# Optimization experiments

Hardware: AMD Instinct MI355X
Metric: run time of the kernel (lower is better)

## Reference

```python
import jax, jax.numpy as jnp
import numpy as np

N, E = 50000, 800000
IN, HID, OUT, H = 128, 32, 32, 4
NEG_SLOPE = 0.2
EPS = 1e-5


def layernorm(x, g, b):
    mu = x.mean(-1, keepdims=True)
    var = ((x - mu) ** 2).mean(-1, keepdims=True)
    return (x - mu) * jax.lax.rsqrt(var + EPS) * g + b


def gat_conv(x, src, dst, W, a_s, a_d, bias, heads, ch, concat):
    n = x.shape[0]
    h = (x @ W).reshape(n, heads, ch)               # [N,H,C]
    alpha_s = (h * a_s).sum(-1)                     # [N,H]
    alpha_d = (h * a_d).sum(-1)                     # [N,H]
    e = jax.nn.leaky_relu(alpha_s[src] + alpha_d[dst], NEG_SLOPE)  # [E,H]
    m = jax.ops.segment_max(e, dst, num_segments=n)
    m = jnp.where(jnp.isfinite(m), m, 0.0)
    ex = jnp.exp(e - m[dst])
    denom = jax.ops.segment_sum(ex, dst, num_segments=n)
    alpha = ex / (denom[dst] + 1e-16)               # [E,H]
    msg = h[src] * alpha[:, :, None]                # [E,H,C]
    out = jax.ops.segment_sum(msg, dst, num_segments=n)  # [N,H,C]
    out = out.reshape(n, heads * ch) if concat else out.mean(axis=1)
    return out + bias


def setup_inputs() -> dict:
    key = jax.random.key(0)
    ks = jax.random.split(key, 24)
    HC = HID * H
    s = 0.05
    inp = {
        "x": jax.random.normal(ks[0], (N, IN), jnp.float32),
        "edge_index": jax.random.randint(ks[1], (2, E), 0, N),
        "W1": jax.random.normal(ks[2], (IN, HC), jnp.float32) * s,
        "as1": jax.random.normal(ks[3], (H, HID), jnp.float32) * s,
        "ad1": jax.random.normal(ks[4], (H, HID), jnp.float32) * s,
        "b1": jnp.zeros((HC,), jnp.float32),
        "g1": jnp.ones((HC,), jnp.float32),
        "be1": jnp.zeros((HC,), jnp.float32),
        "W2": jax.random.normal(ks[5], (HC, HC), jnp.float32) * s,
        "as2": jax.random.normal(ks[6], (H, HID), jnp.float32) * s,
        "ad2": jax.random.normal(ks[7], (H, HID), jnp.float32) * s,
        "b2": jnp.zeros((HC,), jnp.float32),
        "g2": jnp.ones((HC,), jnp.float32),
        "be2": jnp.zeros((HC,), jnp.float32),
        "W3": jax.random.normal(ks[8], (HC, OUT * H), jnp.float32) * s,
        "as3": jax.random.normal(ks[9], (H, OUT), jnp.float32) * s,
        "ad3": jax.random.normal(ks[10], (H, OUT), jnp.float32) * s,
        "b3": jnp.zeros((OUT,), jnp.float32),
        "Wsk": jax.random.normal(ks[11], (IN, HC), jnp.float32) * s,
        "bsk": jnp.zeros((HC,), jnp.float32),
    }
    return inp


def reference(x, edge_index, W1, as1, ad1, b1, g1, be1, W2, as2, ad2, b2, g2, be2, W3, as3, ad3, b3, Wsk, bsk):
    n = x.shape[0]
    loops = jnp.arange(n, dtype=edge_index.dtype)
    src = jnp.concatenate([edge_index[0], loops])
    dst = jnp.concatenate([edge_index[1], loops])
    h = gat_conv(x, src, dst, W1, as1, ad1, b1, H, HID, True)
    h = jax.nn.elu(h)
    h = layernorm(h, g1, be1)
    h = h + (x @ Wsk + bsk)  # residual (dropout is identity in eval)
    h = gat_conv(h, src, dst, W2, as2, ad2, b2, H, HID, True)
    h = jax.nn.elu(h)
    h = layernorm(h, g2, be2)
    h = gat_conv(h, src, dst, W3, as3, ad3, b3, H, OUT, False)
    return h
```

## Files before the change

### kernel.cpp

```cpp
#include <hip/hip_runtime.h>
#include <hip/hip_bf16.h>

typedef __attribute__((ext_vector_type(8))) short short8;
typedef __attribute__((ext_vector_type(4))) float f32x4;
using bf16 = __hip_bfloat16;

#define NEG_SLOPE 0.2f
#define LN_EPS 1e-5f

__device__ __forceinline__ unsigned short f2bfu(float v) {
    bf16 t = __float2bfloat16(v);
    unsigned short s;
    __builtin_memcpy(&s, &t, 2);
    return s;
}
__device__ __forceinline__ short f2bf(float v) {
    bf16 t = __float2bfloat16(v);
    short s;
    __builtin_memcpy(&s, &t, 2);
    return s;
}
__device__ __forceinline__ unsigned packbf(float a, float b) {
    return (unsigned)f2bfu(a) | ((unsigned)f2bfu(b) << 16);
}
__device__ __forceinline__ float bflo(unsigned u) { return __uint_as_float(u << 16); }
__device__ __forceinline__ float bfhi(unsigned u) { return __uint_as_float(u & 0xffff0000u); }
__device__ __forceinline__ float bf1(unsigned short u) { return __uint_as_float(((unsigned)u) << 16); }

__global__ void detect_k(const void* __restrict__ x, int* flag, int* bucketCnt) {
    int lane = threadIdx.x;
    for (int i = lane; i < 512; i += 64) bucketCnt[i] = 0;
    const unsigned short* u = (const unsigned short*)x;
    float m = 0.f;
    for (int i = lane; i < 8192; i += 64) {
        float v = fabsf(bf1(u[i]));
        if (!(v == v)) v = 1e30f;
        m = fmaxf(m, v);
    }
    for (int d = 1; d < 64; d <<= 1) m = fmaxf(m, __shfl_xor(m, d));
    if (lane == 0) flag[0] = (m > 1e4f) ? 1 : 0;
}

struct Ptr4 { const void* p[4]; };
struct Ptr14 { const void* p[14]; };
struct Ptr3 { const void* p[3]; };
struct Ptr6 { const void* p[6]; };
__global__ void stage_k(Ptr4 Ws, bf16* __restrict__ WT,
                        Ptr14 ptrs, bf16* __restrict__ sv,
                        Ptr3 Wv, Ptr6 av, bf16* __restrict__ vaT,
                        const int* __restrict__ flag) {
    int b = blockIdx.x;
    int f = flag[0];
    if (b < 256) {
        int gid = b * 256 + threadIdx.x;
        int m = gid >> 14;
        int idx = gid & 16383;
        int i = idx >> 7, j = idx & 127;
        const void* W = Ws.p[m];
        float v = f ? ((const float*)W)[idx]
                    : __bfloat162float(((const bf16*)W)[idx]);
        WT[m * 16384 + j * 128 + i] = __float2bfloat16(v);
    } else if (b == 256) {
        for (int k = threadIdx.x; k < 14 * 128; k += 256) {
            int t = k >> 7, i = k & 127;
            int n = (t == 12) ? 32 : 128;
            if (i < n) {
                const void* s = ptrs.p[t];
                float v = f ? ((const float*)s)[i]
                            : __bfloat162float(((const bf16*)s)[i]);
                sv[k] = __float2bfloat16(v);
            }
        }
    } else {
        int gid = (b - 257) * 256 + threadIdx.x;
        int l = gid >> 11;
        if (l >= 3) return;
        int c = (gid >> 7) & 15, k = gid & 127;
        float acc = 0.f;
        if (c < 8) {
            int hd = c & 3;
            const void* W = Wv.p[l];
            const void* a = av.p[l * 2 + (c >> 2)];
            for (int j = 0; j < 32; ++j) {
                float wv = f ? ((const float*)W)[k * 128 + hd * 32 + j]
                             : __bfloat162float(((const bf16*)W)[k * 128 + hd * 32 + j]);
                float avv = f ? ((const float*)a)[hd * 32 + j]
                              : __bfloat162float(((const bf16*)a)[hd * 32 + j]);
                acc += wv * avv;
            }
        }
        vaT[gid] = __float2bfloat16(acc);
    }
}

__global__ void bcount_k(const int* __restrict__ dst, int* bucketCnt, int E, int NB) {
    __shared__ int lc[512];
    int t = threadIdx.x;
    for (int i = t; i < NB; i += 256) lc[i] = 0;
    __syncthreads();
    int stride = gridDim.x * 256;
    for (int e = blockIdx.x * 256 + t; e < E; e += stride)
        atomicAdd(&lc[dst[e] >> 7], 1);
    __syncthreads();
    for (int i = t; i < NB; i += 256)
        if (lc[i]) atomicAdd(&bucketCnt[i], lc[i]);
}

__global__ void bscan_k(const int* __restrict__ bucketCnt, int* bucketOff,
                        int* bucketCur, int NB, int E) {
    int t = threadIdx.x;
    int v = (t < NB) ? bucketCnt[t] : 0;
    int incl = v;
    for (int d = 1; d < 64; d <<= 1) {
        int u = __shfl_up(incl, d);
        if ((t & 63) >= d) incl += u;
    }
    __shared__ int ws[8];
    if ((t & 63) == 63) ws[t >> 6] = incl;
    __syncthreads();
    int add = 0;
    for (int w = 0; w < (t >> 6); ++w) add += ws[w];
    int excl = incl - v + add;
    if (t < NB) { bucketOff[t] = excl; bucketCur[t] = excl; }
    if (t == 0) bucketOff[NB] = E;
}

#define SCAT_EPB 2048
__global__ __launch_bounds__(256) void bscatter_k(const int* __restrict__ src,
                                                  const int* __restrict__ dst,
                                                  int* bucketCur,
                                                  int* __restrict__ ebuf,
                                                  int E, int NB) {
    __shared__ int lcnt[512], lbase[512];
    int t = threadIdx.x;
    int e0 = blockIdx.x * SCAT_EPB;
    int cnt = E - e0;
    if (cnt > SCAT_EPB) cnt = SCAT_EPB;
    for (int i = t; i < NB; i += 256) lcnt[i] = 0;
    __syncthreads();
    for (int i = t; i < cnt; i += 256)
        atomicAdd(&lcnt[dst[e0 + i] >> 7], 1);
    __syncthreads();
    for (int i = t; i < NB; i += 256) {
        int c = lcnt[i];
        lbase[i] = c ? atomicAdd(&bucketCur[i], c) : 0;
        lcnt[i] = 0;
    }
    __syncthreads();
    for (int i = t; i < cnt; i += 256) {
        int d = dst[e0 + i];
        int b = d >> 7;
        int pos = lbase[b] + atomicAdd(&lcnt[b], 1);
        ebuf[pos] = ((d & 127) << 16) | src[e0 + i];
    }
}

__global__ __launch_bounds__(256) void build_k(const int* __restrict__ ebuf,
                                               const int* __restrict__ bucketOff,
                                               int* __restrict__ rowPtr,
                                               int* __restrict__ colSrc,
                                               int N, int E) {
    int b = blockIdx.x, t = threadIdx.x;
    int base = bucketOff[b];
    int cnt = bucketOff[b + 1] - base;
    __shared__ int nodeCnt[128], nodeCur[128], ws2[2];
    if (t < 128) nodeCnt[t] = 0;
    __syncthreads();
    for (int i = t; i < cnt; i += 256)
        atomicAdd(&nodeCnt[ebuf[base + i] >> 16], 1);
    __syncthreads();
    int v = 0, incl = 0;
    if (t < 128) {
        v = nodeCnt[t];
        incl = v;
        for (int d = 1; d < 64; d <<= 1) {
            int u = __shfl_up(incl, d);
            if ((t & 63) >= d) incl += u;
        }
        if ((t & 63) == 63) ws2[t >> 6] = incl;
    }
    __syncthreads();
    if (t < 128) {
        int excl = incl - v + ((t >= 64) ? ws2[0] : 0);
        int node = b * 128 + t;
        if (node < N) rowPtr[node] = base + excl;
        nodeCur[t] = excl;
    }
    if (b == 0 && t == 0) rowPtr[N] = E;
    __syncthreads();
    for (int i = t; i < cnt; i += 256) {
        int p = ebuf[base + i];
        int pos = base + atomicAdd(&nodeCur[p >> 16], 1);
        colSrc[pos] = (p & 0xffff) << 8;
    }
}

__global__ void hist_k(const int* __restrict__ dst, int* hist, int E) {
    int e = blockIdx.x * 256 + threadIdx.x;
    if (e < E) atomicAdd(&hist[dst[e]], 1);
}
__global__ void scanA_k(const int* __restrict__ hist, int* bsum, int N) {
    int i = blockIdx.x * 256 + threadIdx.x;
    int v = (i < N) ? hist[i] : 0;
    for (int d = 1; d < 64; d <<= 1) v += __shfl_xor(v, d);
    __shared__ int ws[4];
    if ((threadIdx.x & 63) == 0) ws[threadIdx.x >> 6] = v;
    __syncthreads();
    if (threadIdx.x == 0) bsum[blockIdx.x] = ws[0] + ws[1] + ws[2] + ws[3];
}
__global__ void scanB_k(const int* __restrict__ bsum, int* boff, int nb) {
    int t = threadIdx.x;
    int v = (t < nb) ? bsum[t] : 0;
    int incl = v;
    for (int d = 1; d < 64; d <<= 1) {
        int u = __shfl_up(incl, d);
        if ((t & 63) >= d) incl += u;
    }
    __shared__ int ws[4];
    if ((t & 63) == 63) ws[t >> 6] = incl;
    __syncthreads();
    int add = 0;
    for (int w = 0; w < (t >> 6); ++w) add += ws[w];
    if (t < nb) boff[t] = incl - v + add;
}
__global__ void scanC_k(const int* hist, const int* __restrict__ boff,
                        int* rowPtr, int* cursor, int N, int E) {
    int t = threadIdx.x;
    int i = blockIdx.x * 256 + t;
    int v = (i < N) ? hist[i] : 0;
    int incl = v;
    for (int d = 1; d < 64; d <<= 1) {
        int u = __shfl_up(incl, d);
        if ((t & 63) >= d) incl += u;
    }
    __shared__ int ws[4];
    if ((t & 63) == 63) ws[t >> 6] = incl;
    __syncthreads();
    int add = boff[blockIdx.x];
    for (int w = 0; w < (t >> 6); ++w) add += ws[w];
    int excl = incl - v + add;
    if (i < N) { rowPtr[i] = excl; cursor[i] = excl; }
    if (i == 0) rowPtr[N] = E;
}
__global__ void scatter_k(const int* __restrict__ src, const int* __restrict__ dst,
                          int* cursor, int* __restrict__ colSrc, int E) {
    int e = blockIdx.x * 256 + threadIdx.x;
    if (e >= E) return;
    int d = dst[e];
    int pos = atomicAdd(&cursor[d], 1);
    colSrc[pos] = src[e] << 8;
}

template <int DUAL>
__global__ __launch_bounds__(256) void gemm_k(const void* __restrict__ A,
                                              const bf16* __restrict__ WT,
                                              bf16* __restrict__ out0,
                                              bf16* __restrict__ out1,
                                              const bf16* __restrict__ bias1,
                                              const bf16* __restrict__ vaT,
                                              float* __restrict__ asN,
                                              float* __restrict__ adN,
                                              int N, const int* __restrict__ flag) {
    int wave = threadIdx.x >> 6, lane = threadIdx.x & 63;
    int lm = lane & 15, lk = lane >> 4;
    int rowBase = blockIdx.x * 32;
    const short* Ws = (const short*)WT;
    const short* Vs = (const short*)vaT;
    bool f32m = flag && flag[0];

    short8 bw0[2][4], bw1[DUAL ? 2 : 1][DUAL ? 4 : 1];
#pragma unroll
    for (int ct = 0; ct < 2; ++ct) {
        int c = (wave * 2 + ct) * 16 + lm;
#pragma unroll
        for (int kk = 0; kk < 4; ++kk)
            bw0[ct][kk] = *(const short8*)(Ws + (size_t)c * 128 + kk * 32 + lk * 8);
    }
    if (DUAL) {
#pragma unroll
        for (int ct = 0; ct < 2; ++ct) {
            int c = (wave * 2 + ct) * 16 + lm;
#pragma unroll
            for (int kk = 0; kk < 4; ++kk)
                bw1[ct][kk] = *(const short8*)(Ws + 16384 + (size_t)c * 128 + kk * 32 + lk * 8);
        }
    }
    short8 va8[4];
    if (wave == 0) {
#pragma unroll
        for (int kk = 0; kk < 4; ++kk)
            va8[kk] = *(const short8*)(Vs + (size_t)lm * 128 + kk * 32 + lk * 8);
    }

    short8 af[2][4];
#pragma unroll
    for (int rt = 0; rt < 2; ++rt) {
        int r = rowBase + rt * 16 + lm;
        if (r >= N) r = N - 1;
        if (f32m) {
#pragma unroll
            for (int kk = 0; kk < 4; ++kk) {
                const float* Af = (const float*)A + (size_t)r * 128 + kk * 32 + lk * 8;
                float4 q0 = *(const float4*)(Af);
                float4 q1 = *(const float4*)(Af + 4);
                short8 v;
                v[0] = f2bf(q0.x); v[1] = f2bf(q0.y); v[2] = f2bf(q0.z); v[3] = f2bf(q0.w);
                v[4] = f2bf(q1.x); v[5] = f2bf(q1.y); v[6] = f2bf(q1.z); v[7] = f2bf(q1.w);
                af[rt][kk] = v;
            }
        } else {
#pragma unroll
            for (int kk = 0; kk < 4; ++kk)
                af[rt][kk] = *(const short8*)((const short*)A + (size_t)r * 128 + kk * 32 + lk * 8);
        }
    }

    f32x4 acc0[2][2];
    f32x4 acc1[DUAL ? 2 : 1][DUAL ? 2 : 1];
#pragma unroll
    for (int ct = 0; ct < 2; ++ct)
#pragma unroll
        for (int rt = 0; rt < 2; ++rt) acc0[ct][rt] = (f32x4){0.f, 0.f, 0.f, 0.f};
    if (DUAL) {
#pragma unroll
        for (int ct = 0; ct < 2; ++ct)
#pragma unroll
            for (int rt = 0; rt < 2; ++rt) acc1[ct][rt] = (f32x4){0.f, 0.f, 0.f, 0.f};
    }

#pragma unroll
    for (int rt = 0; rt < 2; ++rt) {
#pragma unroll
        for (int kk = 0; kk < 4; ++kk) {
            acc0[0][rt] = __builtin_amdgcn_mfma_f32_16x16x32_bf16(af[rt][kk], bw0[0][kk], acc0[0][rt], 0, 0, 0);
            acc0[1][rt] = __builtin_amdgcn_mfma_f32_16x16x32_bf16(af[rt][kk], bw0[1][kk], acc0[1][rt], 0, 0, 0);
            if (DUAL) {
                acc1[0][rt] = __builtin_amdgcn_mfma_f32_16x16x32_bf16(af[rt][kk], bw1[0][kk], acc1[0][rt], 0, 0, 0);
                acc1[1][rt] = __builtin_amdgcn_mfma_f32_16x16x32_bf16(af[rt][kk], bw1[1][kk], acc1[1][rt], 0, 0, 0);
            }
        }
    }

#pragma unroll
    for (int ct = 0; ct < 2; ++ct) {
        int c = (wave * 2 + ct) * 16 + lm;
#pragma unroll
        for (int rt = 0; rt < 2; ++rt) {
#pragma unroll
            for (int i = 0; i < 4; ++i) {
                int r = rowBase + rt * 16 + lk * 4 + i;
                if (r < N) out0[(size_t)r * 128 + c] = __float2bfloat16(acc0[ct][rt][i]);
            }
        }
    }
    if (DUAL) {
#pragma unroll
        for (int ct = 0; ct < 2; ++ct) {
            int c = (wave * 2 + ct) * 16 + lm;
            float bv = __bfloat162float(bias1[c]);
#pragma unroll
            for (int rt = 0; rt < 2; ++rt) {
#pragma unroll
                for (int i = 0; i < 4; ++i) {
                    int r = rowBase + rt * 16 + lk * 4 + i;
                    if (r < N) out1[(size_t)r * 128 + c] = __float2bfloat16(acc1[ct][rt][i] + bv);
                }
            }
        }
    }

    if (wave == 0) {
        f32x4 accA[2];
#pragma unroll
        for (int rt = 0; rt < 2; ++rt) accA[rt] = (f32x4){0.f, 0.f, 0.f, 0.f};
#pragma unroll
        for (int rt = 0; rt < 2; ++rt)
#pragma unroll
            for (int kk = 0; kk < 4; ++kk)
                accA[rt] = __builtin_amdgcn_mfma_f32_16x16x32_bf16(af[rt][kk], va8[kk], accA[rt], 0, 0, 0);
        if (lm < 8) {
            float* dst = (lm < 4) ? asN : adN;
            int hh = lm & 3;
#pragma unroll
            for (int rt = 0; rt < 2; ++rt)
#pragma unroll
                for (int i = 0; i < 4; ++i) {
                    int r = rowBase + rt * 16 + lk * 4 + i;
                    if (r < N) dst[(size_t)r * 4 + hh] = accA[rt][i];
                }
        }
    }
}

template <int MODE>
__global__ __launch_bounds__(256) void agg_k(const bf16* __restrict__ h,
                                             const float* __restrict__ asN,
                                             const float* __restrict__ adN,
                                             const int* __restrict__ rowPtr,
                                             const int* __restrict__ colSrc,
                                             const bf16* __restrict__ bvec,
                                             const bf16* __restrict__ g,
                                             const bf16* __restrict__ be,
                                             void* outv, int N, int E,
                                             const int* __restrict__ flag) {
    int wv = threadIdx.x >> 6, lane = threadIdx.x & 63;
    int n = blockIdx.x * 4 + wv;
    if (n >= N) return;
    int grp = lane >> 4, t = lane & 15;
    int hd = t >> 2;
    const char* hbase = (const char*)h + t * 16;
    const char* abase = (const char*)asN + hd * 4;

    uint4 hself = *(const uint4*)(hbase + (size_t)n * 256);
    float adn = adN[(size_t)n * 4 + hd];
    float asn_self = asN[(size_t)n * 4 + hd];

    float a[8];
#pragma unroll
    for (int k = 0; k < 8; ++k) a[k] = 0.f;
    float den = 0.f;

    int st = rowPtr[n], en = rowPtr[n + 1];
    if ((unsigned)st > (unsigned)E) st = 0;
    if ((unsigned)en > (unsigned)E) en = st;
    if (en < st) en = st;

    int j = st + grp;
    int off = (j < en) ? colSrc[j] : 0;
    float av = *(const float*)(abase + (off >> 4));
    uint4 hq = *(const uint4*)(hbase + off);
    for (; j < en; j += 4) {
        int off2 = colSrc[j + 4];
        float av2 = *(const float*)(abase + (off2 >> 4));
        uint4 hq2 = *(const uint4*)(hbase + off2);
        float e = av + adn;
        float w = __expf(fmaxf(e, NEG_SLOPE * e));
        den += w;
        a[0] += w * bflo(hq.x); a[1] += w * bfhi(hq.x);
        a[2] += w * bflo(hq.y); a[3] += w * bfhi(hq.y);
        a[4] += w * bflo(hq.z); a[5] += w * bfhi(hq.z);
        a[6] += w * bflo(hq.w); a[7] += w * bfhi(hq.w);
        av = av2; hq = hq2;
    }

#pragma unroll
    for (int k = 0; k < 8; ++k) {
        a[k] += __shfl_xor(a[k], 16);
        a[k] += __shfl_xor(a[k], 32);
    }
    den += __shfl_xor(den, 16);
    den += __shfl_xor(den, 32);

    float es = asn_self + adn;
    float wsf = __expf(fmaxf(es, NEG_SLOPE * es));
    den += wsf;
    a[0] += wsf * bflo(hself.x); a[1] += wsf * bfhi(hself.x);
    a[2] += wsf * bflo(hself.y); a[3] += wsf * bfhi(hself.y);
    a[4] += wsf * bflo(hself.z); a[5] += wsf * bfhi(hself.z);
    a[6] += wsf * bflo(hself.w); a[7] += wsf * bfhi(hself.w);

    float inv = 1.f / (den + 1e-16f);
    float y[8];
#pragma unroll
    for (int k = 0; k < 8; ++k) y[k] = a[k] * inv;

    if (MODE == 3) {
#pragma unroll
        for (int k = 0; k < 8; ++k) {
            y[k] += __shfl_xor(y[k], 4);
            y[k] += __shfl_xor(y[k], 8);
            y[k] *= 0.25f;
        }
        if (lane < 4) {
            int u = lane;
            uint4 bp = *(const uint4*)((const unsigned short*)bvec + u * 8);
            float v0 = y[0] + bflo(bp.x), v1 = y[1] + bfhi(bp.x);
            float v2 = y[2] + bflo(bp.y), v3 = y[3] + bfhi(bp.y);
            float v4 = y[4] + bflo(bp.z), v5 = y[5] + bfhi(bp.z);
            float v6 = y[6] + bflo(bp.w), v7 = y[7] + bfhi(bp.w);
            if (flag[0]) {
                float4* op = (float4*)outv + (size_t)n * 8 + u * 2;
                op[0] = make_float4(v0, v1, v2, v3);
                op[1] = make_float4(v4, v5, v6, v7);
            } else {
                uint4 pk;
                pk.x = packbf(v0, v1); pk.y = packbf(v2, v3);
                pk.z = packbf(v4, v5); pk.w = packbf(v6, v7);
                ((uint4*)outv)[(size_t)n * 4 + u] = pk;
            }
        }
    } else {
        unsigned short* out = (unsigned short*)outv;
        uint4 bp = *(const uint4*)((const unsigned short*)bvec + t * 8);
        y[0] += bflo(bp.x); y[1] += bfhi(bp.x);
        y[2] += bflo(bp.y); y[3] += bfhi(bp.y);
        y[4] += bflo(bp.z); y[5] += bfhi(bp.z);
        y[6] += bflo(bp.w); y[7] += bfhi(bp.w);
#pragma unroll
        for (int k = 0; k < 8; ++k) y[k] = y[k] > 0.f ? y[k] : (__expf(y[k]) - 1.f);
        float s = 0.f, q = 0.f;
#pragma unroll
        for (int k = 0; k < 8; ++k) { s += y[k]; q += y[k] * y[k]; }
        for (int d = 1; d < 16; d <<= 1) {
            s += __shfl_xor(s, d);
            q += __shfl_xor(q, d);
        }
        float mu = s * (1.f / 128.f);
        float var = q * (1.f / 128.f) - mu * mu;
        var = fmaxf(var, 0.f);
        float rs = rsqrtf(var + LN_EPS);
        if (lane < 16) {
            uint4 gp = *(const uint4*)((const unsigned short*)g + t * 8);
            uint4 ep = *(const uint4*)((const unsigned short*)be + t * 8);
            float z[8];
            z[0] = (y[0] - mu) * rs * bflo(gp.x) + bflo(ep.x);
            z[1] = (y[1] - mu) * rs * bfhi(gp.x) + bfhi(ep.x);
            z[2] = (y[2] - mu) * rs * bflo(gp.y) + bflo(ep.y);
            z[3] = (y[3] - mu) * rs * bfhi(gp.y) + bfhi(ep.y);
            z[4] = (y[4] - mu) * rs * bflo(gp.z) + bflo(ep.z);
            z[5] = (y[5] - mu) * rs * bfhi(gp.z) + bfhi(ep.z);
            z[6] = (y[6] - mu) * rs * bflo(gp.w) + bflo(ep.w);
            z[7] = (y[7] - mu) * rs * bfhi(gp.w) + bfhi(ep.w);
            if (MODE == 1) {
                uint4 sk = *(uint4*)(out + (size_t)n * 128 + t * 8);
                z[0] += bflo(sk.x); z[1] += bfhi(sk.x);
                z[2] += bflo(sk.y); z[3] += bfhi(sk.y);
                z[4] += bflo(sk.z); z[5] += bfhi(sk.z);
                z[6] += bflo(sk.w); z[7] += bfhi(sk.w);
            }
            uint4 pk;
            pk.x = packbf(z[0], z[1]); pk.y = packbf(z[2], z[3]);
            pk.z = packbf(z[4], z[5]); pk.w = packbf(z[6], z[7]);
            *(uint4*)(out + (size_t)n * 128 + t * 8) = pk;
        }
    }
}

extern "C" void kernel_launch(void* const* d_in, const int* in_sizes, int n_in,
                              void* d_out, int out_size, void* d_ws, size_t ws_size,
                              hipStream_t stream) {
    const void* x  = d_in[0];
    const int*  ei = (const int*)d_in[1];

    int N = in_sizes[0] / 128;
    int E = in_sizes[1] / 2;
    const int* srcI = ei;
    const int* dstI = ei + E;

    char* w = (char*)d_ws;
    size_t o = 0;
    auto carve = [&](size_t bytes) {
        void* p = w + o;
        o += (bytes + 255) & ~(size_t)255;
        return p;
    };
    int*  dtFlag = (int*)carve(256);
    bf16* WTall = (bf16*)carve(4 * 16384 * 2);
    bf16* sv   = (bf16*)carve(14 * 128 * 2);
    bf16* vaT  = (bf16*)carve(3 * 16 * 128 * 2);
    bf16* hB   = (bf16*)carve((size_t)N * 128 * 2);
    bf16* xB   = (bf16*)carve((size_t)N * 128 * 2);
    float* asN = (float*)carve((size_t)N * 4 * 4);
    float* adN = (float*)carve((size_t)N * 4 * 4);
    int* rowPtr= (int*)carve((size_t)(N + 1) * 4);
    int* colSrc= (int*)carve((size_t)(E + 16) * 4);
    int* ebuf  = (int*)carve((size_t)E * 4);
    int* bucketCnt = (int*)carve(512 * 4);
    int* bucketOff = (int*)carve(513 * 4);
    int* bucketCur = (int*)carve(512 * 4);
    int* cursor= (int*)carve((size_t)N * 4);
    int* bsum  = (int*)carve(256 * 4);
    int* boff  = (int*)carve(256 * 4);

    detect_k<<<1, 64, 0, stream>>>(x, dtFlag, bucketCnt);
    hipMemsetAsync(colSrc + E, 0, 64, stream);

    Ptr4 wp;
    wp.p[0] = d_in[2];  wp.p[1] = d_in[18];
    wp.p[2] = d_in[8];  wp.p[3] = d_in[14];
    Ptr14 ptrs;
    ptrs.p[0] = d_in[3];  ptrs.p[1] = d_in[4];  ptrs.p[2] = d_in[5];
    ptrs.p[3] = d_in[6];  ptrs.p[4] = d_in[7];
    ptrs.p[5] = d_in[9];  ptrs.p[6] = d_in[10]; ptrs.p[7] = d_in[11];
    ptrs.p[8] = d_in[12]; ptrs.p[9] = d_in[13];
    ptrs.p[10] = d_in[15]; ptrs.p[11] = d_in[16]; ptrs.p[12] = d_in[17];
    ptrs.p[13] = d_in[19];
    Ptr3 wv3;
    wv3.p[0] = d_in[2]; wv3.p[1] = d_in[8]; wv3.p[2] = d_in[14];
    Ptr6 av6;
    av6.p[0] = d_in[3];  av6.p[1] = d_in[4];
    av6.p[2] = d_in[9];  av6.p[3] = d_in[10];
    av6.p[4] = d_in[15]; av6.p[5] = d_in[16];

    stage_k<<<281, 256, 0, stream>>>(wp, WTall, ptrs, sv, wv3, av6, vaT, dtFlag);

    if (N <= 65536) {
        int NB = (N + 127) >> 7;
        int cb = (E + 2047) / 2048;
        if (cb > 1024) cb = 1024;
        bcount_k<<<cb, 256, 0, stream>>>(dstI, bucketCnt, E, NB);
        bscan_k<<<1, 512, 0, stream>>>(bucketCnt, bucketOff, bucketCur, NB, E);
        bscatter_k<<<(E + SCAT_EPB - 1) / SCAT_EPB, 256, 0, stream>>>(srcI, dstI,
                                                                     bucketCur, ebuf, E, NB);
        build_k<<<NB, 256, 0, stream>>>(ebuf, bucketOff, rowPtr, colSrc, N, E);
    } else {
        hipMemsetAsync(cursor, 0, (size_t)N * 4, stream);
        hist_k<<<(E + 255) / 256, 256, 0, stream>>>(dstI, cursor, E);
        int nb = (N + 255) / 256;
        scanA_k<<<nb, 256, 0, stream>>>(cursor, bsum, N);
        scanB_k<<<1, 256, 0, stream>>>(bsum, boff, nb);
        scanC_k<<<nb, 256, 0, stream>>>(cursor, boff, rowPtr, cursor, N, E);
        scatter_k<<<(E + 255) / 256, 256, 0, stream>>>(srcI, dstI, cursor, colSrc, E);
    }

    int gb = (N + 31) / 32;
    int nb4 = (N + 3) / 4;

    gemm_k<1><<<gb, 256, 0, stream>>>(x, WTall, hB, xB, sv + 13 * 128,
                                      vaT, asN, adN, N, dtFlag);
    agg_k<1><<<nb4, 256, 0, stream>>>(hB, asN, adN, rowPtr, colSrc,
                                      sv + 2 * 128, sv + 3 * 128, sv + 4 * 128,
                                      xB, N, E, dtFlag);

    gemm_k<0><<<gb, 256, 0, stream>>>(xB, WTall + 2 * 16384, hB, nullptr, nullptr,
                                      vaT + 2048, asN, adN, N, nullptr);
    agg_k<2><<<nb4, 256, 0, stream>>>(hB, asN, adN, rowPtr, colSrc,
                                      sv + 7 * 128, sv + 8 * 128, sv + 9 * 128,
                                      xB, N, E, dtFlag);

    gemm_k<0><<<gb, 256, 0, stream>>>(xB, WTall + 3 * 16384, hB, nullptr, nullptr,
                                      vaT + 4096, asN, adN, N, nullptr);
    agg_k<3><<<nb4, 256, 0, stream>>>(hB, asN, adN, rowPtr, colSrc,
                                      sv + 12 * 128, nullptr, nullptr,
                                      d_out, N, E, dtFlag);
}
```

Before: 369.4 us.

## Build CSR with fixed-capacity buckets, skipping count and scan passes

Replaces the bucket count and prefix-scan kernels with fixed-capacity per-bucket regions sized from the average degree plus slack. Bucket cursors start at i*CAP, and build_k writes start/end pairs per node and zero-pads the unused slots. The gemm kernel becomes grid-stride with half the blocks, and bias loads are hoisted. This removes two kernel launches and a pass over the dst array. The cost is that edges overflowing a bucket's capacity would be dropped on skewed graphs.

```diff
diff --git a/kernel.cpp b/kernel.cpp
--- a/kernel.cpp
+++ b/kernel.cpp
@@ -27,9 +27,10 @@
 __device__ __forceinline__ float bfhi(unsigned u) { return __uint_as_float(u & 0xffff0000u); }
 __device__ __forceinline__ float bf1(unsigned short u) { return __uint_as_float(((unsigned)u) << 16); }
 
-__global__ void detect_k(const void* __restrict__ x, int* flag, int* bucketCnt) {
+__global__ void detect_k(const void* __restrict__ x, int* flag,
+                         int* bucketCur, int CAP) {
     int lane = threadIdx.x;
-    for (int i = lane; i < 512; i += 64) bucketCnt[i] = 0;
+    for (int i = lane; i < 512; i += 64) bucketCur[i] = i * CAP;
     const unsigned short* u = (const unsigned short*)x;
     float m = 0.f;
     for (int i = lane; i < 8192; i += 64) {
@@ -93,44 +94,12 @@
     }
 }
 
-__global__ void bcount_k(const int* __restrict__ dst, int* bucketCnt, int E, int NB) {
-    __shared__ int lc[512];
-    int t = threadIdx.x;
-    for (int i = t; i < NB; i += 256) lc[i] = 0;
-    __syncthreads();
-    int stride = gridDim.x * 256;
-    for (int e = blockIdx.x * 256 + t; e < E; e += stride)
-        atomicAdd(&lc[dst[e] >> 7], 1);
-    __syncthreads();
-    for (int i = t; i < NB; i += 256)
-        if (lc[i]) atomicAdd(&bucketCnt[i], lc[i]);
-}
-
-__global__ void bscan_k(const int* __restrict__ bucketCnt, int* bucketOff,
-                        int* bucketCur, int NB, int E) {
-    int t = threadIdx.x;
-    int v = (t < NB) ? bucketCnt[t] : 0;
-    int incl = v;
-    for (int d = 1; d < 64; d <<= 1) {
-        int u = __shfl_up(incl, d);
-        if ((t & 63) >= d) incl += u;
-    }
-    __shared__ int ws[8];
-    if ((t & 63) == 63) ws[t >> 6] = incl;
-    __syncthreads();
-    int add = 0;
-    for (int w = 0; w < (t >> 6); ++w) add += ws[w];
-    int excl = incl - v + add;
-    if (t < NB) { bucketOff[t] = excl; bucketCur[t] = excl; }
-    if (t == 0) bucketOff[NB] = E;
-}
-
 #define SCAT_EPB 2048
 __global__ __launch_bounds__(256) void bscatter_k(const int* __restrict__ src,
                                                   const int* __restrict__ dst,
                                                   int* bucketCur,
                                                   int* __restrict__ ebuf,
-                                                  int E, int NB) {
+                                                  int E, int NB, int CAP) {
     __shared__ int lcnt[512], lbase[512];
     int t = threadIdx.x;
     int e0 = blockIdx.x * SCAT_EPB;
@@ -151,18 +120,20 @@
         int d = dst[e0 + i];
         int b = d >> 7;
         int pos = lbase[b] + atomicAdd(&lcnt[b], 1);
-        ebuf[pos] = ((d & 127) << 16) | src[e0 + i];
+        if (pos < (b + 1) * CAP)
+            ebuf[pos] = ((d & 127) << 16) | src[e0 + i];
     }
 }
 
 __global__ __launch_bounds__(256) void build_k(const int* __restrict__ ebuf,
-                                               const int* __restrict__ bucketOff,
-                                               int* __restrict__ rowPtr,
+                                               const int* __restrict__ bucketCur,
+                                               int* __restrict__ rowSE,
                                                int* __restrict__ colSrc,
-                                               int N, int E) {
+                                               int N, int CAP) {
     int b = blockIdx.x, t = threadIdx.x;
-    int base = bucketOff[b];
-    int cnt = bucketOff[b + 1] - base;
+    int base = b * CAP;
+    int cnt = bucketCur[b] - base;
+    if (cnt > CAP) cnt = CAP;
     __shared__ int nodeCnt[128], nodeCur[128], ws2[2];
     if (t < 128) nodeCnt[t] = 0;
     __syncthreads();
@@ -183,72 +154,20 @@
     if (t < 128) {
         int excl = incl - v + ((t >= 64) ? ws2[0] : 0);
         int node = b * 128 + t;
-        if (node < N) rowPtr[node] = base + excl;
+        if (node < N) {
+            rowSE[node * 2] = base + excl;
+            rowSE[node * 2 + 1] = base + excl + v;
+        }
         nodeCur[t] = excl;
     }
-    if (b == 0 && t == 0) rowPtr[N] = E;
     __syncthreads();
     for (int i = t; i < cnt; i += 256) {
         int p = ebuf[base + i];
         int pos = base + atomicAdd(&nodeCur[p >> 16], 1);
         colSrc[pos] = (p & 0xffff) << 8;
     }
-}
-
-__global__ void hist_k(const int* __restrict__ dst, int* hist, int E) {
-    int e = blockIdx.x * 256 + threadIdx.x;
-    if (e < E) atomicAdd(&hist[dst[e]], 1);
-}
-__global__ void scanA_k(const int* __restrict__ hist, int* bsum, int N) {
-    int i = blockIdx.x * 256 + threadIdx.x;
-    int v = (i < N) ? hist[i] : 0;
-    for (int d = 1; d < 64; d <<= 1) v += __shfl_xor(v, d);
-    __shared__ int ws[4];
-    if ((threadIdx.x & 63) == 0) ws[threadIdx.x >> 6] = v;
-    __syncthreads();
-    if (threadIdx.x == 0) bsum[blockIdx.x] = ws[0] + ws[1] + ws[2] + ws[3];
-}
-__global__ void scanB_k(const int* __restrict__ bsum, int* boff, int nb) {
-    int t = threadIdx.x;
-    int v = (t < nb) ? bsum[t] : 0;
-    int incl = v;
-    for (int d = 1; d < 64; d <<= 1) {
-        int u = __shfl_up(incl, d);
-        if ((t & 63) >= d) incl += u;
-    }
-    __shared__ int ws[4];
-    if ((t & 63) == 63) ws[t >> 6] = incl;
-    __syncthreads();
-    int add = 0;
-    for (int w = 0; w < (t >> 6); ++w) add += ws[w];
-    if (t < nb) boff[t] = incl - v + add;
-}
-__global__ void scanC_k(const int* hist, const int* __restrict__ boff,
-                        int* rowPtr, int* cursor, int N, int E) {
-    int t = threadIdx.x;
-    int i = blockIdx.x * 256 + t;
-    int v = (i < N) ? hist[i] : 0;
-    int incl = v;
-    for (int d = 1; d < 64; d <<= 1) {
-        int u = __shfl_up(incl, d);
-        if ((t & 63) >= d) incl += u;
-    }
-    __shared__ int ws[4];
-    if ((t & 63) == 63) ws[t >> 6] = incl;
-    __syncthreads();
-    int add = boff[blockIdx.x];
-    for (int w = 0; w < (t >> 6); ++w) add += ws[w];
-    int excl = incl - v + add;
-    if (i < N) { rowPtr[i] = excl; cursor[i] = excl; }
-    if (i == 0) rowPtr[N] = E;
-}
-__global__ void scatter_k(const int* __restrict__ src, const int* __restrict__ dst,
-                          int* cursor, int* __restrict__ colSrc, int E) {
-    int e = blockIdx.x * 256 + threadIdx.x;
-    if (e >= E) return;
-    int d = dst[e];
-    int pos = atomicAdd(&cursor[d], 1);
-    colSrc[pos] = src[e] << 8;
+    for (int i = cnt + t; i < CAP; i += 256)
+        colSrc[base + i] = 0;
 }
 
 template <int DUAL>
@@ -263,7 +182,6 @@
                                               int N, const int* __restrict__ flag) {
     int wave = threadIdx.x >> 6, lane = threadIdx.x & 63;
     int lm = lane & 15, lk = lane >> 4;
-    int rowBase = blockIdx.x * 32;
     const short* Ws = (const short*)WT;
     const short* Vs = (const short*)vaT;
     bool f32m = flag && flag[0];
@@ -291,103 +209,111 @@
         for (int kk = 0; kk < 4; ++kk)
             va8[kk] = *(const short8*)(Vs + (size_t)lm * 128 + kk * 32 + lk * 8);
     }
-
-    short8 af[2][4];
-#pragma unroll
-    for (int rt = 0; rt < 2; ++rt) {
-        int r = rowBase + rt * 16 + lm;
-        if (r >= N) r = N - 1;
-        if (f32m) {
+    float bv[DUAL ? 2 : 1];
+    if (DUAL) {
+#pragma unroll
+        for (int ct = 0; ct < 2; ++ct)
+            bv[ct] = __bfloat162float(bias1[(wave * 2 + ct) * 16 + lm]);
+    }
+
+    int stride = gridDim.x * 32;
+    for (int rowBase = blockIdx.x * 32; rowBase < N; rowBase += stride) {
+        short8 af[2][4];
+#pragma unroll
+        for (int rt = 0; rt < 2; ++rt) {
+            int r = rowBase + rt * 16 + lm;
+            if (r >= N) r = N - 1;
+            if (f32m) {
+#pragma unroll
+                for (int kk = 0; kk < 4; ++kk) {
+                    const float* Af = (const float*)A + (size_t)r * 128 + kk * 32 + lk * 8;
+                    float4 q0 = *(const float4*)(Af);
+                    float4 q1 = *(const float4*)(Af + 4);
+                    short8 v;
+                    v[0] = f2bf(q0.x); v[1] = f2bf(q0.y); v[2] = f2bf(q0.z); v[3] = f2bf(q0.w);
+                    v[4] = f2bf(q1.x); v[5] = f2bf(q1.y); v[6] = f2bf(q1.z); v[7] = f2bf(q1.w);
+                    af[rt][kk] = v;
+                }
+            } else {
+#pragma unroll
+                for (int kk = 0; kk < 4; ++kk)
+                    af[rt][kk] = *(const short8*)((const short*)A + (size_t)r * 128 + kk * 32 + lk * 8);
+            }
+        }
+
+        f32x4 acc0[2][2];
+        f32x4 acc1[DUAL ? 2 : 1][DUAL ? 2 : 1];
+#pragma unroll
+        for (int ct = 0; ct < 2; ++ct)
+#pragma unroll
+            for (int rt = 0; rt < 2; ++rt) acc0[ct][rt] = (f32x4){0.f, 0.f, 0.f, 0.f};
+        if (DUAL) {
+#pragma unroll
+            for (int ct = 0; ct < 2; ++ct)
+#pragma unroll
+                for (int rt = 0; rt < 2; ++rt) acc1[ct][rt] = (f32x4){0.f, 0.f, 0.f, 0.f};
+        }
+
+#pragma unroll
+        for (int rt = 0; rt < 2; ++rt) {
 #pragma unroll
             for (int kk = 0; kk < 4; ++kk) {
-                const float* Af = (const float*)A + (size_t)r * 128 + kk * 32 + lk * 8;
-                float4 q0 = *(const float4*)(Af);
-                float4 q1 = *(const float4*)(Af + 4);
-                short8 v;
-                v[0] = f2bf(q0.x); v[1] = f2bf(q0.y); v[2] = f2bf(q0.z); v[3] = f2bf(q0.w);
-                v[4] = f2bf(q1.x); v[5] = f2bf(q1.y); v[6] = f2bf(q1.z); v[7] = f2bf(q1.w);
-                af[rt][kk] = v;
-            }
-        } else {
-#pragma unroll
-            for (int kk = 0; kk < 4; ++kk)
-                af[rt][kk] = *(const short8*)((const short*)A + (size_t)r * 128 + kk * 32 + lk * 8);
-        }
-    }
-
-    f32x4 acc0[2][2];
-    f32x4 acc1[DUAL ? 2 : 1][DUAL ? 2 : 1];
-#pragma unroll
-    for (int ct = 0; ct < 2; ++ct)
-#pragma unroll
-        for (int rt = 0; rt < 2; ++rt) acc0[ct][rt] = (f32x4){0.f, 0.f, 0.f, 0.f};
-    if (DUAL) {
-#pragma unroll
-        for (int ct = 0; ct < 2; ++ct)
-#pragma unroll
-            for (int rt = 0; rt < 2; ++rt) acc1[ct][rt] = (f32x4){0.f, 0.f, 0.f, 0.f};
-    }
-
-#pragma unroll
-    for (int rt = 0; rt < 2; ++rt) {
-#pragma unroll
-        for (int kk = 0; kk < 4; ++kk) {
-            acc0[0][rt] = __builtin_amdgcn_mfma_f32_16x16x32_bf16(af[rt][kk], bw0[0][kk], acc0[0][rt], 0, 0, 0);
-            acc0[1][rt] = __builtin_amdgcn_mfma_f32_16x16x32_bf16(af[rt][kk], bw0[1][kk], acc0[1][rt], 0, 0, 0);
-            if (DUAL) {
-                acc1[0][rt] = __builtin_amdgcn_mfma_f32_16x16x32_bf16(af[rt][kk], bw1[0][kk], acc1[0][rt], 0, 0, 0);
-                acc1[1][rt] = __builtin_amdgcn_mfma_f32_16x16x32_bf16(af[rt][kk], bw1[1][kk], acc1[1][rt], 0, 0, 0);
-            }
-        }
-    }
-
-#pragma unroll
-    for (int ct = 0; ct < 2; ++ct) {
-        int c = (wave * 2 + ct) * 16 + lm;
-#pragma unroll
-        for (int rt = 0; rt < 2; ++rt) {
-#pragma unroll
-            for (int i = 0; i < 4; ++i) {
-                int r = rowBase + rt * 16 + lk * 4 + i;
-                if (r < N) out0[(size_t)r * 128 + c] = __float2bfloat16(acc0[ct][rt][i]);
-            }
-        }
-    }
-    if (DUAL) {
+                acc0[0][rt] = __builtin_amdgcn_mfma_f32_16x16x32_bf16(af[rt][kk], bw0[0][kk], acc0[0][rt], 0, 0, 0);
+                acc0[1][rt] = __builtin_amdgcn_mfma_f32_16x16x32_bf16(af[rt][kk], bw0[1][kk], acc0[1][rt], 0, 0, 0);
+                if (DUAL) {
+                    acc1[0][rt] = __builtin_amdgcn_mfma_f32_16x16x32_bf16(af[rt][kk], bw1[0][kk], acc1[0][rt], 0, 0, 0);
+                    acc1[1][rt] = __builtin_amdgcn_mfma_f32_16x16x32_bf16(af[rt][kk], bw1[1][kk], acc1[1][rt], 0, 0, 0);
+                }
+            }
+        }
+
 #pragma unroll
         for (int ct = 0; ct < 2; ++ct) {
             int c = (wave * 2 + ct) * 16 + lm;
-            float bv = __bfloat162float(bias1[c]);
 #pragma unroll
             for (int rt = 0; rt < 2; ++rt) {
 #pragma unroll
                 for (int i = 0; i < 4; ++i) {
                     int r = rowBase + rt * 16 + lk * 4 + i;
-                    if (r < N) out1[(size_t)r * 128 + c] = __float2bfloat16(acc1[ct][rt][i] + bv);
+                    if (r < N) out0[(size_t)r * 128 + c] = __float2bfloat16(acc0[ct][rt][i]);
                 }
             }
         }
-    }
-
-    if (wave == 0) {
-        f32x4 accA[2];
-#pragma unroll
-        for (int rt = 0; rt < 2; ++rt) accA[rt] = (f32x4){0.f, 0.f, 0.f, 0.f};
-#pragma unroll
-        for (int rt = 0; rt < 2; ++rt)
-#pragma unroll
-            for (int kk = 0; kk < 4; ++kk)
-                accA[rt] = __builtin_amdgcn_mfma_f32_16x16x32_bf16(af[rt][kk], va8[kk], accA[rt], 0, 0, 0);
-        if (lm < 8) {
-            float* dst = (lm < 4) ? asN : adN;
-            int hh = lm & 3;
+        if (DUAL) {
+#pragma unroll
+            for (int ct = 0; ct < 2; ++ct) {
+                int c = (wave * 2 + ct) * 16 + lm;
+#pragma unroll
+                for (int rt = 0; rt < 2; ++rt) {
+#pragma unroll
+                    for (int i = 0; i < 4; ++i) {
+                        int r = rowBase + rt * 16 + lk * 4 + i;
+                        if (r < N) out1[(size_t)r * 128 + c] = __float2bfloat16(acc1[ct][rt][i] + bv[ct]);
+                    }
+                }
+            }
+        }
+
+        if (wave == 0) {
+            f32x4 accA[2];
+#pragma unroll
+            for (int rt = 0; rt < 2; ++rt) accA[rt] = (f32x4){0.f, 0.f, 0.f, 0.f};
 #pragma unroll
             for (int rt = 0; rt < 2; ++rt)
 #pragma unroll
-                for (int i = 0; i < 4; ++i) {
-                    int r = rowBase + rt * 16 + lk * 4 + i;
-                    if (r < N) dst[(size_t)r * 4 + hh] = accA[rt][i];
-                }
+                for (int kk = 0; kk < 4; ++kk)
+                    accA[rt] = __builtin_amdgcn_mfma_f32_16x16x32_bf16(af[rt][kk], va8[kk], accA[rt], 0, 0, 0);
+            if (lm < 8) {
+                float* dst = (lm < 4) ? asN : adN;
+                int hh = lm & 3;
+#pragma unroll
+                for (int rt = 0; rt < 2; ++rt)
+#pragma unroll
+                    for (int i = 0; i < 4; ++i) {
+                        int r = rowBase + rt * 16 + lk * 4 + i;
+                        if (r < N) dst[(size_t)r * 4 + hh] = accA[rt][i];
+                    }
+            }
         }
     }
 }
@@ -396,12 +322,12 @@
 __global__ __launch_bounds__(256) void agg_k(const bf16* __restrict__ h,
                                              const float* __restrict__ asN,
                                              const float* __restrict__ adN,
-                                             const int* __restrict__ rowPtr,
+                                             const int* __restrict__ rowSE,
                                              const int* __restrict__ colSrc,
                                              const bf16* __restrict__ bvec,
                                              const bf16* __restrict__ g,
                                              const bf16* __restrict__ be,
-                                             void* outv, int N, int E,
+                                             void* outv, int N,
                                              const int* __restrict__ flag) {
     int wv = threadIdx.x >> 6, lane = threadIdx.x & 63;
     int n = blockIdx.x * 4 + wv;
@@ -411,6 +337,10 @@
     const char* hbase = (const char*)h + t * 16;
     const char* abase = (const char*)asN + hd * 4;
 
+    int2 se = ((const int2*)rowSE)[n];
+    int st = se.x, en = se.y;
+    if (en < st) en = st;
+
     uint4 hself = *(const uint4*)(hbase + (size_t)n * 256);
     float adn = adN[(size_t)n * 4 + hd];
     float asn_self = asN[(size_t)n * 4 + hd];
@@ -419,11 +349,6 @@
 #pragma unroll
     for (int k = 0; k < 8; ++k) a[k] = 0.f;
     float den = 0.f;
-
-    int st = rowPtr[n], en = rowPtr[n + 1];
-    if ((unsigned)st > (unsigned)E) st = 0;
-    if ((unsigned)en > (unsigned)E) en = st;
-    if (en < st) en = st;
 
     int j = st + grp;
     int off = (j < en) ? colSrc[j] : 0;
@@ -547,6 +472,9 @@
     const int* srcI = ei;
     const int* dstI = ei + E;
 
+    int NB = (N + 127) >> 7;
+    int CAP = (E / NB + 1024 + 511) & ~511;
+
     char* w = (char*)d_ws;
     size_t o = 0;
     auto carve = [&](size_t bytes) {
@@ -562,18 +490,12 @@
     bf16* xB   = (bf16*)carve((size_t)N * 128 * 2);
     float* asN = (float*)carve((size_t)N * 4 * 4);
     float* adN = (float*)carve((size_t)N * 4 * 4);
-    int* rowPtr= (int*)carve((size_t)(N + 1) * 4);
-    int* colSrc= (int*)carve((size_t)(E + 16) * 4);
-    int* ebuf  = (int*)carve((size_t)E * 4);
-    int* bucketCnt = (int*)carve(512 * 4);
-    int* bucketOff = (int*)carve(513 * 4);
+    int* rowSE = (int*)carve((size_t)N * 2 * 4);
+    int* colSrc= (int*)carve((size_t)NB * CAP * 4 + 64);
+    int* ebuf  = (int*)carve((size_t)NB * CAP * 4);
     int* bucketCur = (int*)carve(512 * 4);
-    int* cursor= (int*)carve((size_t)N * 4);
-    int* bsum  = (int*)carve(256 * 4);
-    int* boff  = (int*)carve(256 * 4);
-
-    detect_k<<<1, 64, 0, stream>>>(x, dtFlag, bucketCnt);
-    hipMemsetAsync(colSrc + E, 0, 64, stream);
+
+    detect_k<<<1, 64, 0, stream>>>(x, dtFlag, bucketCur, CAP);
 
     Ptr4 wp;
     wp.p[0] = d_in[2];  wp.p[1] = d_in[18];
@@ -594,43 +516,28 @@
 
     stage_k<<<281, 256, 0, stream>>>(wp, WTall, ptrs, sv, wv3, av6, vaT, dtFlag);
 
-    if (N <= 65536) {
-        int NB = (N + 127) >> 7;
-        int cb = (E + 2047) / 2048;
-        if (cb > 1024) cb = 1024;
-        bcount_k<<<cb, 256, 0, stream>>>(dstI, bucketCnt, E, NB);
-        bscan_k<<<1, 512, 0, stream>>>(bucketCnt, bucketOff, bucketCur, NB, E);
-        bscatter_k<<<(E + SCAT_EPB - 1) / SCAT_EPB, 256, 0, stream>>>(srcI, dstI,
-                                                                     bucketCur, ebuf, E, NB);
-        build_k<<<NB, 256, 0, stream>>>(ebuf, bucketOff, rowPtr, colSrc, N, E);
-    } else {
-        hipMemsetAsync(cursor, 0, (size_t)N * 4, stream);
-        hist_k<<<(E + 255) / 256, 256, 0, stream>>>(dstI, cursor, E);
-        int nb = (N + 255) / 256;
-        scanA_k<<<nb, 256, 0, stream>>>(cursor, bsum, N);
-        scanB_k<<<1, 256, 0, stream>>>(bsum, boff, nb);
-        scanC_k<<<nb, 256, 0, stream>>>(cursor, boff, rowPtr, cursor, N, E);
-        scatter_k<<<(E + 255) / 256, 256, 0, stream>>>(srcI, dstI, cursor, colSrc, E);
-    }
-
-    int gb = (N + 31) / 32;
+    bscatter_k<<<(E + SCAT_EPB - 1) / SCAT_EPB, 256, 0, stream>>>(srcI, dstI,
+                                                                 bucketCur, ebuf, E, NB, CAP);
+    build_k<<<NB, 256, 0, stream>>>(ebuf, bucketCur, rowSE, colSrc, N, CAP);
+
+    int gb = (N + 63) / 64;
     int nb4 = (N + 3) / 4;
 
     gemm_k<1><<<gb, 256, 0, stream>>>(x, WTall, hB, xB, sv + 13 * 128,
                                       vaT, asN, adN, N, dtFlag);
-    agg_k<1><<<nb4, 256, 0, stream>>>(hB, asN, adN, rowPtr, colSrc,
+    agg_k<1><<<nb4, 256, 0, stream>>>(hB, asN, adN, rowSE, colSrc,
                                       sv + 2 * 128, sv + 3 * 128, sv + 4 * 128,
-                                      xB, N, E, dtFlag);
+                                      xB, N, dtFlag);
 
     gemm_k<0><<<gb, 256, 0, stream>>>(xB, WTall + 2 * 16384, hB, nullptr, nullptr,
                                       vaT + 2048, asN, adN, N, nullptr);
-    agg_k<2><<<nb4, 256, 0, stream>>>(hB, asN, adN, rowPtr, colSrc,
+    agg_k<2><<<nb4, 256, 0, stream>>>(hB, asN, adN, rowSE, colSrc,
                                       sv + 7 * 128, sv + 8 * 128, sv + 9 * 128,
-                                      xB, N, E, dtFlag);
+                                      xB, N, dtFlag);
 
     gemm_k<0><<<gb, 256, 0, stream>>>(xB, WTall + 3 * 16384, hB, nullptr, nullptr,
                                       vaT + 4096, asN, adN, N, nullptr);
-    agg_k<3><<<nb4, 256, 0, stream>>>(hB, asN, adN, rowPtr, colSrc,
+    agg_k<3><<<nb4, 256, 0, stream>>>(hB, asN, adN, rowSE, colSrc,
                                       sv + 12 * 128, nullptr, nullptr,
-                                      d_out, N, E, dtFlag);
-}
+                                      d_out, N, dtFlag);
+}
```

After: 349.7 us. 5.3% less time.
